# Kernel optimization log

Measured on AMD Instinct MI355X. Metric: run time of the kernel, lower is better.

Reference implementation:

```python
import jax, jax.numpy as jnp
import numpy as np

B = 1024      # batch of seed nodes
S = 16        # sample_size
H = 256       # hidden
IN = 150      # in_dim + NUM_CLASS (128 + 22)
OUT = 22
HEADS = 8
NN = 100000   # number of graph nodes
LN_EPS = 1e-5


def setup_inputs() -> dict:
    key = jax.random.key(0)
    ks = jax.random.split(key, 16)
    sc = 0.05
    return {
        "node_feats": jax.random.normal(ks[0], (NN, IN), jnp.float32),
        "batch": jax.random.randint(ks[1], (B,), 0, NN),
        "nbr2": jax.random.randint(ks[2], (B, S), 0, NN),
        "nbr1": jax.random.randint(ks[3], (B * (S + 1), S), 0, NN),
        "W_in": jax.random.normal(ks[4], (IN, H), jnp.float32) * sc,
        "b_in": jnp.zeros((H,), jnp.float32),
        "Wqkv": jax.random.normal(ks[5], (2, 3, H, H), jnp.float32) * sc,
        "bqkv": jnp.zeros((2, 3, H), jnp.float32),
        "Wo": jax.random.normal(ks[6], (2, H, H), jnp.float32) * sc,
        "bo": jnp.zeros((2, H), jnp.float32),
        "Wf": jax.random.normal(ks[7], (2, H, H), jnp.float32) * sc,
        "bf": jnp.zeros((2, H), jnp.float32),
        "ln_g": jnp.ones((4, H), jnp.float32),
        "ln_b": jnp.zeros((4, H), jnp.float32),
        "W_out": jax.random.normal(ks[8], (H, OUT), jnp.float32) * sc,
        "b_out": jnp.zeros((OUT,), jnp.float32),
    }


def _layer_norm(x, g, b):
    m = jnp.mean(x, axis=-1, keepdims=True)
    v = jnp.mean((x - m) ** 2, axis=-1, keepdims=True)
    return (x - m) * jax.lax.rsqrt(v + LN_EPS) * g + b


def _mha(q, kv, Wq, Wk, Wv, bq, bk, bv, Wout, bout):
    # q: [N, 1, H], kv: [N, S, H]; single-query multi-head attention
    N, Sk, _ = kv.shape
    dh = H // HEADS
    qp = (q @ Wq + bq).reshape(N, 1, HEADS, dh)
    kp = (kv @ Wk + bk).reshape(N, Sk, HEADS, dh)
    vp = (kv @ Wv + bv).reshape(N, Sk, HEADS, dh)
    att = jax.nn.softmax(
        jnp.einsum("nqhd,nkhd->nhqk", qp, kp) / np.float32(np.sqrt(dh)), axis=-1
    )
    o = jnp.einsum("nhqk,nkhd->nqhd", att, vp).reshape(N, 1, H)
    return o @ Wout + bout


def _attn_block(x, l, Wqkv, bqkv, Wo, bo, Wf, bf, ln_g, ln_b):
    # x: [N, S+1, H]; slot 0 is the query (self), rest are sampled neighbors
    q, kv = x[:, 0:1, :], x[:, 1:, :]
    h = _mha(q, kv, Wqkv[l, 0], Wqkv[l, 1], Wqkv[l, 2],
             bqkv[l, 0], bqkv[l, 1], bqkv[l, 2], Wo[l], bo[l])
    h = h[:, 0, :] + q[:, 0, :]                       # residual
    h = _layer_norm(h, ln_g[2 * l], ln_b[2 * l])
    h = h + (h @ Wf[l] + bf[l])                       # FFN (single Linear) + residual
    return _layer_norm(h, ln_g[2 * l + 1], ln_b[2 * l + 1])


def reference(node_feats, batch, nbr2, nbr1, W_in, b_in, Wqkv, bqkv, Wo, bo,
              Wf, bf, ln_g, ln_b, W_out, b_out):
    # Recursive neighbor expansion (unrolled for layers=2)
    ids1 = jnp.concatenate([batch[:, None], nbr2], axis=1).reshape(-1)   # [B*(S+1)]
    ids0 = jnp.concatenate([ids1[:, None], nbr1], axis=1).reshape(-1)    # [B*(S+1)^2]
    # layer 0: proj_in(features) = ReLU(Linear) (Dropout identity in eval)
    h0 = jax.nn.relu(node_feats[ids0] @ W_in + b_in)                     # [M0, H]
    # layer 1
    h1 = _attn_block(h0.reshape(B * (S + 1), S + 1, H), 0,
                     Wqkv, bqkv, Wo, bo, Wf, bf, ln_g, ln_b)
    # layer 2
    h2 = _attn_block(h1.reshape(B, S + 1, H), 1,
                     Wqkv, bqkv, Wo, bo, Wf, bf, ln_g, ln_b)
    # proj_out: Linear -> Softmax
    return jax.nn.softmax(h2 @ W_out + b_out, axis=-1)
```

## Files before the change

kernel.cpp:

```cpp
#include <hip/hip_runtime.h>
#include <hip/hip_bf16.h>
#include <math.h>

typedef unsigned short ushort_t;
typedef __bf16 bf16x8 __attribute__((ext_vector_type(8)));
typedef float  f32x4  __attribute__((ext_vector_type(4)));
typedef __attribute__((address_space(1))) const unsigned int* gas_t;
typedef __attribute__((address_space(3))) unsigned int* las_t;

#define B_SZ   1024
#define SEQ    17
#define KVN    16
#define HDIM   256
#define NHEAD  8
#define DH     32
#define INF    150
#define OUTD   22
#define LN_EPS 1e-5f
#define N1     (B_SZ * SEQ)
#define NN_    100000
#define NKV2   782
#define NHQ2   136

constexpr size_t SZ_H0    = (size_t)NN_ * 256 * 2;
constexpr size_t SZ_KV0   = (size_t)NN_ * 512 * 2;
constexpr size_t SZ_ROW   = (size_t)N1 * 256 * 2;
constexpr size_t OFF_HQ   = 0;
constexpr size_t OFF_KV0  = OFF_HQ + SZ_H0;
constexpr size_t OFF_QKV1 = OFF_KV0;
constexpr size_t OFF_O1   = OFF_QKV1 + (size_t)N1 * 768 * 2;
constexpr size_t OFF_H2   = OFF_O1 + (size_t)B_SZ * 256 * 2;
constexpr size_t OFF_Q0   = OFF_KV0 + SZ_KV0;
constexpr size_t OFF_O0   = OFF_Q0 + SZ_ROW;
constexpr size_t OFF_H1   = OFF_O0;
constexpr size_t OFF_IDS  = OFF_O0 + SZ_ROW;
constexpr size_t OFF_WTIN = OFF_IDS + (size_t)N1 * 4;
constexpr size_t OFF_WKV0 = OFF_WTIN + 256 * 160 * 2;
constexpr size_t OFF_WQ0  = OFF_WKV0 + 512 * 256 * 2;
constexpr size_t OFF_WKVQ1= OFF_WQ0 + 256 * 256 * 2;
constexpr size_t OFF_WO0  = OFF_WKVQ1 + 768 * 256 * 2;
constexpr size_t OFF_WF0  = OFF_WO0 + 256 * 256 * 2;
constexpr size_t OFF_WO1  = OFF_WF0 + 256 * 256 * 2;
constexpr size_t OFF_WF1  = OFF_WO1 + 256 * 256 * 2;
constexpr size_t OFF_B1   = OFF_WF1 + 256 * 256 * 2;

__device__ __forceinline__ ushort_t f2bfu(float x) {
    __hip_bfloat16 h = __float2bfloat16(x);
    return *reinterpret_cast<ushort_t*>(&h);
}
__device__ __forceinline__ float bfu2f(ushort_t u) {
    __hip_bfloat16 h;
    *reinterpret_cast<ushort_t*>(&h) = u;
    return __bfloat162float(h);
}
__device__ __forceinline__ f32x4 mfma16(bf16x8 a, bf16x8 b, f32x4 c) {
    return __builtin_amdgcn_mfma_f32_16x16x32_bf16(a, b, c, 0, 0, 0);
}

__device__ __forceinline__ void stage_b512(
    const ushort_t* __restrict__ Bsrc, int Kld, int kk,
    ushort_t* lbase, int w, int lane) {
    #pragma unroll
    for (int i = 0; i < 2; ++i) {
        int inst = w * 2 + i;
        int row = inst * 16 + (lane >> 2);
        int q_log = (lane & 3) ^ ((row >> 1) & 3);
        const ushort_t* src = Bsrc + (size_t)row * Kld + kk + q_log * 8;
        __builtin_amdgcn_global_load_lds((gas_t)(const void*)src,
                                         (las_t)(void*)(lbase + inst * 512),
                                         16, 0, 0);
    }
}

__global__ __launch_bounds__(256) void k_prep(
    const float* __restrict__ W_in, const float* __restrict__ Wqkv,
    const float* __restrict__ Wo, const float* __restrict__ Wf,
    const float* __restrict__ bqkv,
    const int* __restrict__ batch, const int* __restrict__ nbr2,
    char* __restrict__ ws) {
    const int job = blockIdx.y;
    const int idx = blockIdx.x * 256 + threadIdx.x;
    if (job == 11) {
        if (idx < N1) {
            int b = idx / SEQ, s = idx % SEQ;
            ((int*)(ws + OFF_IDS))[idx] = (s == 0) ? batch[b] : nbr2[b * KVN + s - 1];
        }
        return;
    }
    if (job == 12) {
        if (idx < 768) ((float*)(ws + OFF_B1))[idx] = bqkv[768 + ((idx + 256) % 768)];
        return;
    }
    const float* src = nullptr; ushort_t* dst = nullptr;
    int Kpad = 256, Kvalid = 256;
    switch (job) {
        case 0:  src = W_in;           dst = (ushort_t*)(ws + OFF_WTIN); Kpad = 160; Kvalid = 150; break;
        case 1:  src = Wqkv + 65536;   dst = (ushort_t*)(ws + OFF_WKV0); break;
        case 2:  src = Wqkv + 131072;  dst = (ushort_t*)(ws + OFF_WKV0) + 65536; break;
        case 3:  src = Wqkv;           dst = (ushort_t*)(ws + OFF_WQ0); break;
        case 4:  src = Wqkv + 262144;  dst = (ushort_t*)(ws + OFF_WKVQ1); break;
        case 5:  src = Wqkv + 327680;  dst = (ushort_t*)(ws + OFF_WKVQ1) + 65536; break;
        case 6:  src = Wqkv + 196608;  dst = (ushort_t*)(ws + OFF_WKVQ1) + 131072; break;
        case 7:  src = Wo;             dst = (ushort_t*)(ws + OFF_WO0); break;
        case 8:  src = Wo + 65536;     dst = (ushort_t*)(ws + OFF_WO1); break;
        case 9:  src = Wf;             dst = (ushort_t*)(ws + OFF_WF0); break;
        case 10: src = Wf + 65536;     dst = (ushort_t*)(ws + OFF_WF1); break;
    }
    const int total = 256 * Kpad;
    if (idx >= total) return;
    int n = idx / Kpad, k = idx % Kpad;
    dst[idx] = (k < Kvalid) ? f2bfu(src[(size_t)k * 256 + n]) : (ushort_t)0;
}

__global__ __launch_bounds__(512) void k_fused(
    const float* __restrict__ nf,
    const ushort_t* __restrict__ Wt_in, const float* __restrict__ b_in,
    const ushort_t* __restrict__ Wkv, const ushort_t* __restrict__ Wq,
    const float* __restrict__ bqkv, const int* __restrict__ ids1,
    ushort_t* __restrict__ kv0, ushort_t* __restrict__ hq,
    ushort_t* __restrict__ q0) {
    __shared__ ushort_t Ah[128 * 256];
    __shared__ ushort_t Bst[8192];
    const int tid = threadIdx.x;
    const bool iskv = blockIdx.x < NKV2;
    const int m0 = (iskv ? blockIdx.x : blockIdx.x - NKV2) * 128;
    const int lane = tid & 63, w = tid >> 6;
    const int wr = w >> 2, wc = w & 3;
    const int lr = lane & 15, q4 = lane >> 4, lk = q4 * 8;

    {
        ushort_t (*Astage)[168] = reinterpret_cast<ushort_t (*)[168]>(Ah);
        #pragma unroll
        for (int i = 0; i < 5; ++i) {
            int flat = tid + i * 512;
            int row = flat / 20, ch = flat % 20;
            int gm;
            if (iskv) { gm = m0 + row; if (gm >= NN_) gm = 0; }
            else      { gm = ids1[m0 + row]; }
            const float* ap = nf + (size_t)gm * INF + ch * 8;
            ushort_t tmp[8];
            if (ch < 18) {
                #pragma unroll
                for (int j = 0; j < 4; ++j) {
                    float2 f = *reinterpret_cast<const float2*>(ap + j * 2);
                    tmp[j * 2] = f2bfu(f.x); tmp[j * 2 + 1] = f2bfu(f.y);
                }
            } else {
                #pragma unroll
                for (int j = 0; j < 8; ++j) {
                    int k = ch * 8 + j;
                    tmp[j] = (k < INF) ? f2bfu(ap[j]) : (ushort_t)0;
                }
            }
            *reinterpret_cast<int4*>(&Astage[row][ch * 8]) = *reinterpret_cast<int4*>(tmp);
        }
    }
    __syncthreads();

    f32x4 acc1[4][4] = {};
    {
        ushort_t (*Astage)[168] = reinterpret_cast<ushort_t (*)[168]>(Ah);
        for (int s = 0; s < 5; ++s) {
            __builtin_amdgcn_s_barrier();
            stage_b512(Wt_in, 160, s * 32, Bst, w, lane);
            __syncthreads();
            bf16x8 a[4], b[4];
            #pragma unroll
            for (int mi = 0; mi < 4; ++mi)
                a[mi] = *reinterpret_cast<const bf16x8*>(
                    &Astage[wr * 64 + mi * 16 + lr][s * 32 + lk]);
            #pragma unroll
            for (int ni = 0; ni < 4; ++ni) {
                int n = wc * 64 + ni * 16 + lr;
                b[ni] = *reinterpret_cast<const bf16x8*>(
                    &Bst[n * 32 + ((q4 ^ ((n >> 1) & 3)) * 8)]);
            }
            #pragma unroll
            for (int mi = 0; mi < 4; ++mi)
                #pragma unroll
                for (int ni = 0; ni < 4; ++ni)
                    acc1[mi][ni] = mfma16(a[mi], b[ni], acc1[mi][ni]);
        }
    }
    __syncthreads();

    #pragma unroll
    for (int ni = 0; ni < 4; ++ni) {
        int col = wc * 64 + ni * 16 + lr;
        float bb = b_in[col];
        #pragma unroll
        for (int mi = 0; mi < 4; ++mi)
            #pragma unroll
            for (int r = 0; r < 4; ++r) {
                int row = wr * 64 + mi * 16 + q4 * 4 + r;
                Ah[row * 256 + (col ^ ((row & 7) << 3))] =
                    f2bfu(fmaxf(acc1[mi][ni][r] + bb, 0.f));
            }
    }
    __syncthreads();

    if (!iskv) {
        #pragma unroll
        for (int i = 0; i < 8; ++i) {
            int flat = tid + i * 512;
            int row = flat >> 5, ch = flat & 31;
            *reinterpret_cast<int4*>(hq + (size_t)(m0 + row) * 256 + ch * 8) =
                *reinterpret_cast<const int4*>(&Ah[row * 256 + ((ch ^ (row & 7)) * 8)]);
        }
    }

    const int npass = iskv ? 2 : 1;
    for (int h = 0; h < npass; ++h) {
        const ushort_t* Bm = iskv ? (Wkv + (size_t)h * 65536) : Wq;
        const float* bias = iskv ? (bqkv + 256 + h * 256) : bqkv;
        f32x4 acc2[4][4] = {};
        for (int s = 0; s < 8; ++s) {
            __builtin_amdgcn_s_barrier();
            stage_b512(Bm, 256, s * 32, Bst, w, lane);
            __syncthreads();
            bf16x8 a[4], b[4];
            #pragma unroll
            for (int mi = 0; mi < 4; ++mi) {
                int row = wr * 64 + mi * 16 + lr;
                int chunk = (s * 4 + q4) ^ (row & 7);
                a[mi] = *reinterpret_cast<const bf16x8*>(&Ah[row * 256 + chunk * 8]);
            }
            #pragma unroll
            for (int ni = 0; ni < 4; ++ni) {
                int n = wc * 64 + ni * 16 + lr;
                b[ni] = *reinterpret_cast<const bf16x8*>(
                    &Bst[n * 32 + ((q4 ^ ((n >> 1) & 3)) * 8)]);
            }
            #pragma unroll
            for (int mi = 0; mi < 4; ++mi)
                #pragma unroll
                for (int ni = 0; ni < 4; ++ni)
                    acc2[mi][ni] = mfma16(a[mi], b[ni], acc2[mi][ni]);
        }
        ushort_t* outp = iskv ? kv0 : q0;
        const int ldo = iskv ? 512 : 256;
        const int coff = (iskv ? h * 256 : 0) + wc * 64;
        #pragma unroll
        for (int ni = 0; ni < 4; ++ni) {
            float bb = bias[wc * 64 + ni * 16 + lr];
            #pragma unroll
            for (int mi = 0; mi < 4; ++mi)
                #pragma unroll
                for (int r = 0; r < 4; ++r) {
                    int grow = m0 + wr * 64 + mi * 16 + q4 * 4 + r;
                    if (!iskv || grow < NN_)
                        outp[(size_t)grow * ldo + coff + ni * 16 + lr] =
                            f2bfu(acc2[mi][ni][r] + bb);
                }
        }
    }
}

__global__ __launch_bounds__(256) void k_ffn(
    const ushort_t* __restrict__ Ain, const ushort_t* __restrict__ W1t,
    const float* __restrict__ b1,
    const ushort_t* __restrict__ resmat, int rstride,
    const float* __restrict__ lng1, const float* __restrict__ lnb1,
    const ushort_t* __restrict__ W2t, const float* __restrict__ b2,
    const float* __restrict__ lng2, const float* __restrict__ lnb2,
    ushort_t* __restrict__ out,
    const ushort_t* __restrict__ Wqkv1t, const float* __restrict__ bqkv1,
    ushort_t* __restrict__ qkvout) {
    __shared__ ushort_t Al[32][264];
    __shared__ float xr[32][260];
    __shared__ float mrow[32], rrow[32];
    const int tid = threadIdx.x;
    const int m0 = blockIdx.x * 32;
    const int lane = tid & 63, w = tid >> 6;
    const int lr = lane & 15, q4 = lane >> 4, lk = q4 * 8;

    #pragma unroll
    for (int j = 0; j < 4; ++j) {
        int flat = tid + j * 256;
        int row = flat >> 5, ch = flat & 31;
        *reinterpret_cast<int4*>(&Al[row][ch * 8]) =
            *reinterpret_cast<const int4*>(Ain + (size_t)(m0 + row) * 256 + ch * 8);
    }
    __syncthreads();

    f32x4 acc[2][4];
    #pragma unroll
    for (int g = 0; g < 2; ++g) {
        const ushort_t* Wt = g ? W2t : W1t;
        #pragma unroll
        for (int mi = 0; mi < 2; ++mi)
            #pragma unroll
            for (int ni = 0; ni < 4; ++ni) acc[mi][ni] = f32x4{0.f, 0.f, 0.f, 0.f};
        bf16x8 bc[4];
        #pragma unroll
        for (int ni = 0; ni < 4; ++ni)
            bc[ni] = *reinterpret_cast<const bf16x8*>(
                Wt + (size_t)(w * 64 + ni * 16 + lr) * 256 + lk);
        #pragma unroll
        for (int s = 0; s < 8; ++s) {
            bf16x8 bn[4];
            if (s < 7) {
                #pragma unroll
                for (int ni = 0; ni < 4; ++ni)
                    bn[ni] = *reinterpret_cast<const bf16x8*>(
                        Wt + (size_t)(w * 64 + ni * 16 + lr) * 256 + (s + 1) * 32 + lk);
            }
            bf16x8 a0 = *reinterpret_cast<const bf16x8*>(&Al[lr][s * 32 + lk]);
            bf16x8 a1 = *reinterpret_cast<const bf16x8*>(&Al[16 + lr][s * 32 + lk]);
            #pragma unroll
            for (int ni = 0; ni < 4; ++ni) {
                acc[0][ni] = mfma16(a0, bc[ni], acc[0][ni]);
                acc[1][ni] = mfma16(a1, bc[ni], acc[1][ni]);
            }
            if (s < 7) {
                #pragma unroll
                for (int ni = 0; ni < 4; ++ni) bc[ni] = bn[ni];
            }
        }
        #pragma unroll
        for (int mi = 0; mi < 2; ++mi)
            #pragma unroll
            for (int ni = 0; ni < 4; ++ni)
                #pragma unroll
                for (int r = 0; r < 4; ++r)
                    xr[mi * 16 + q4 * 4 + r][w * 64 + ni * 16 + lr] = acc[mi][ni][r];
        __syncthreads();
        {
            float bb = g ? b2[tid] : b1[tid];
            if (g == 0) {
                for (int r = 0; r < 32; ++r)
                    xr[r][tid] += bb + bfu2f(resmat[(size_t)(m0 + r) * rstride * 256 + tid]);
            } else {
                for (int r = 0; r < 32; ++r)
                    xr[r][tid] += bb + bfu2f(Al[r][tid]);
            }
        }
        __syncthreads();
        for (int rr = w * 8; rr < w * 8 + 8; ++rr) {
            float4 v = *reinterpret_cast<const float4*>(&xr[rr][lane * 4]);
            float s1 = v.x + v.y + v.z + v.w;
            float s2 = v.x * v.x + v.y * v.y + v.z * v.z + v.w * v.w;
            #pragma unroll
            for (int off = 32; off > 0; off >>= 1) {
                s1 += __shfl_xor(s1, off);
                s2 += __shfl_xor(s2, off);
            }
            if (lane == 0) {
                float m = s1 * (1.f / 256.f);
                float var = s2 * (1.f / 256.f) - m * m;
                mrow[rr] = m;
                rrow[rr] = rsqrtf(var + LN_EPS);
            }
        }
        __syncthreads();
        if (g == 0) {
            float gg = lng1[tid], bb = lnb1[tid];
            for (int r = 0; r < 32; ++r)
                Al[r][tid] = f2bfu((xr[r][tid] - mrow[r]) * rrow[r] * gg + bb);
        } else {
            float gg = lng2[tid], bb = lnb2[tid];
            for (int r = 0; r < 32; ++r) {
                float v = (xr[r][tid] - mrow[r]) * rrow[r] * gg + bb;
                ushort_t uv = f2bfu(v);
                out[(size_t)(m0 + r) * 256 + tid] = uv;
                if (qkvout) Al[r][tid] = uv;
            }
        }
        __syncthreads();
    }

    if (qkvout) {
        for (int p = 0; p < 3; ++p) {
            #pragma unroll
            for (int mi = 0; mi < 2; ++mi)
                #pragma unroll
                for (int ni = 0; ni < 4; ++ni) acc[mi][ni] = f32x4{0.f, 0.f, 0.f, 0.f};
            const ushort_t* Wt = Wqkv1t + (size_t)p * 256 * 256;
            bf16x8 bc[4];
            #pragma unroll
            for (int ni = 0; ni < 4; ++ni)
                bc[ni] = *reinterpret_cast<const bf16x8*>(
                    Wt + (size_t)(w * 64 + ni * 16 + lr) * 256 + lk);
            #pragma unroll
            for (int s = 0; s < 8; ++s) {
                bf16x8 bn[4];
                if (s < 7) {
                    #pragma unroll
                    for (int ni = 0; ni < 4; ++ni)
                        bn[ni] = *reinterpret_cast<const bf16x8*>(
                            Wt + (size_t)(w * 64 + ni * 16 + lr) * 256 + (s + 1) * 32 + lk);
                }
                bf16x8 a0 = *reinterpret_cast<const bf16x8*>(&Al[lr][s * 32 + lk]);
                bf16x8 a1 = *reinterpret_cast<const bf16x8*>(&Al[16 + lr][s * 32 + lk]);
                #pragma unroll
                for (int ni = 0; ni < 4; ++ni) {
                    acc[0][ni] = mfma16(a0, bc[ni], acc[0][ni]);
                    acc[1][ni] = mfma16(a1, bc[ni], acc[1][ni]);
                }
                if (s < 7) {
                    #pragma unroll
                    for (int ni = 0; ni < 4; ++ni) bc[ni] = bn[ni];
                }
            }
            #pragma unroll
            for (int ni = 0; ni < 4; ++ni) {
                int col = w * 64 + ni * 16 + lr;
                float bb = bqkv1[p * 256 + col];
                #pragma unroll
                for (int mi = 0; mi < 2; ++mi)
                    #pragma unroll
                    for (int r = 0; r < 4; ++r) {
                        int row = m0 + mi * 16 + q4 * 4 + r;
                        qkvout[(size_t)row * 768 + p * 256 + col] =
                            f2bfu(acc[mi][ni][r] + bb);
                    }
            }
        }
    }
}

__global__ __launch_bounds__(256) void attn_wave(
    const ushort_t* __restrict__ q_all, int qld, int qoff, int qstride,
    const ushort_t* __restrict__ kv_all, int kvld, int koff, int voff,
    const int* __restrict__ kvidx, int ngroups, ushort_t* __restrict__ o_out) {
    __shared__ ushort_t KL[4][KVN][264];
    __shared__ ushort_t VL[4][KVN][264];
    const int w = threadIdx.x >> 6, lane = threadIdx.x & 63;
    const int g = blockIdx.x * 4 + w;
    if (g >= ngroups) return;

    int idx16 = 0;
    if (lane < KVN)
        idx16 = kvidx ? kvidx[g * KVN + lane] : g * SEQ + 1 + lane;

    float qv[4];
    {
        uint2 u = *reinterpret_cast<const uint2*>(
            q_all + (size_t)g * qstride * qld + qoff + lane * 4);
        qv[0] = bfu2f((ushort_t)(u.x & 0xffff));
        qv[1] = bfu2f((ushort_t)(u.x >> 16));
        qv[2] = bfu2f((ushort_t)(u.y & 0xffff));
        qv[3] = bfu2f((ushort_t)(u.y >> 16));
    }
    {
        const int r = lane & 15, qtr = lane >> 4;
        int rid = __shfl(idx16, r);
        const ushort_t* kb = kv_all + (size_t)rid * kvld + koff;
        const ushort_t* vb = kv_all + (size_t)rid * kvld + voff;
        #pragma unroll
        for (int j = 0; j < 8; ++j) {
            int c8 = (qtr * 8 + j) * 8;
            *reinterpret_cast<int4*>(&KL[w][r][c8]) = *reinterpret_cast<const int4*>(kb + c8);
            *reinterpret_cast<int4*>(&VL[w][r][c8]) = *reinterpret_cast<const int4*>(vb + c8);
        }
    }
    float att[KVN];
    #pragma unroll
    for (int k = 0; k < KVN; ++k) {
        uint2 u = *reinterpret_cast<const uint2*>(&KL[w][k][lane * 4]);
        float p = qv[0] * bfu2f((ushort_t)(u.x & 0xffff))
                + qv[1] * bfu2f((ushort_t)(u.x >> 16))
                + qv[2] * bfu2f((ushort_t)(u.y & 0xffff))
                + qv[3] * bfu2f((ushort_t)(u.y >> 16));
        p += __shfl_xor(p, 1);
        p += __shfl_xor(p, 2);
        p += __shfl_xor(p, 4);
        att[k] = p * 0.17677669529663687f;
    }
    float m = att[0];
    #pragma unroll
    for (int k = 1; k < KVN; ++k) m = fmaxf(m, att[k]);
    float sum = 0.f;
    #pragma unroll
    for (int k = 0; k < KVN; ++k) { att[k] = __expf(att[k] - m); sum += att[k]; }
    float inv = 1.f / sum;
    float o[4] = {0.f, 0.f, 0.f, 0.f};
    #pragma unroll
    for (int k = 0; k < KVN; ++k) {
        uint2 u = *reinterpret_cast<const uint2*>(&VL[w][k][lane * 4]);
        float a = att[k] * inv;
        o[0] += a * bfu2f((ushort_t)(u.x & 0xffff));
        o[1] += a * bfu2f((ushort_t)(u.x >> 16));
        o[2] += a * bfu2f((ushort_t)(u.y & 0xffff));
        o[3] += a * bfu2f((ushort_t)(u.y >> 16));
    }
    uint2 r;
    r.x = (unsigned)f2bfu(o[0]) | ((unsigned)f2bfu(o[1]) << 16);
    r.y = (unsigned)f2bfu(o[2]) | ((unsigned)f2bfu(o[3]) << 16);
    *reinterpret_cast<uint2*>(o_out + (size_t)g * 256 + lane * 4) = r;
}

__global__ __launch_bounds__(64) void k_out(
    const ushort_t* __restrict__ h2, const float* __restrict__ W_out,
    const float* __restrict__ b_out, float* __restrict__ out) {
    const int b = blockIdx.x, j = threadIdx.x;
    __shared__ float xr[HDIM];
    for (int k = j; k < HDIM; k += 64) xr[k] = bfu2f(h2[(size_t)b * HDIM + k]);
    __syncthreads();
    float logit = -1e30f;
    if (j < OUTD) {
        float acc = b_out[j];
        for (int k = 0; k < HDIM; ++k) acc += xr[k] * W_out[k * OUTD + j];
        logit = acc;
    }
    float m = logit;
    #pragma unroll
    for (int off = 32; off > 0; off >>= 1) m = fmaxf(m, __shfl_xor(m, off));
    float e = (j < OUTD) ? __expf(logit - m) : 0.f;
    float s = e;
    #pragma unroll
    for (int off = 32; off > 0; off >>= 1) s += __shfl_xor(s, off);
    if (j < OUTD) out[(size_t)b * OUTD + j] = e / s;
}

extern "C" void kernel_launch(void* const* d_in, const int* in_sizes, int n_in,
                              void* d_out, int out_size, void* d_ws, size_t ws_size,
                              hipStream_t stream) {
    const float* nf    = (const float*)d_in[0];
    const int*   batch = (const int*)d_in[1];
    const int*   nbr2  = (const int*)d_in[2];
    const int*   nbr1  = (const int*)d_in[3];
    const float* W_in  = (const float*)d_in[4];
    const float* b_in  = (const float*)d_in[5];
    const float* Wqkv  = (const float*)d_in[6];
    const float* bqkv  = (const float*)d_in[7];
    const float* Wo    = (const float*)d_in[8];
    const float* bo    = (const float*)d_in[9];
    const float* Wf    = (const float*)d_in[10];
    const float* bf    = (const float*)d_in[11];
    const float* ln_g  = (const float*)d_in[12];
    const float* ln_b  = (const float*)d_in[13];
    const float* W_out = (const float*)d_in[14];
    const float* b_out = (const float*)d_in[15];
    float* out = (float*)d_out;
    char* ws = (char*)d_ws;

    ushort_t* hq   = (ushort_t*)(ws + OFF_HQ);
    ushort_t* kv0  = (ushort_t*)(ws + OFF_KV0);
    ushort_t* q0   = (ushort_t*)(ws + OFF_Q0);
    ushort_t* o0   = (ushort_t*)(ws + OFF_O0);
    ushort_t* h1   = (ushort_t*)(ws + OFF_H1);
    ushort_t* qkv1 = (ushort_t*)(ws + OFF_QKV1);
    ushort_t* o1   = (ushort_t*)(ws + OFF_O1);
    ushort_t* h2   = (ushort_t*)(ws + OFF_H2);
    const int* ids1 = (const int*)(ws + OFF_IDS);

    hipLaunchKernelGGL(k_prep, dim3(256, 13), dim3(256), 0, stream,
                       W_in, Wqkv, Wo, Wf, bqkv, batch, nbr2, ws);
    hipLaunchKernelGGL(k_fused, dim3(NKV2 + NHQ2), dim3(512), 0, stream,
                       nf, (const ushort_t*)(ws + OFF_WTIN), b_in,
                       (const ushort_t*)(ws + OFF_WKV0),
                       (const ushort_t*)(ws + OFF_WQ0), bqkv, ids1,
                       kv0, hq, q0);
    hipLaunchKernelGGL(attn_wave, dim3(N1 / 4), dim3(256), 0, stream,
                       q0, 256, 0, 1, kv0, 512, 0, 256, nbr1, N1, o0);
    hipLaunchKernelGGL(k_ffn, dim3(N1 / 32), dim3(256), 0, stream,
                       o0, (const ushort_t*)(ws + OFF_WO0), bo,
                       hq, 1, ln_g, ln_b,
                       (const ushort_t*)(ws + OFF_WF0), bf,
                       ln_g + 256, ln_b + 256, h1,
                       (const ushort_t*)(ws + OFF_WKVQ1),
                       (const float*)(ws + OFF_B1), qkv1);
    hipLaunchKernelGGL(attn_wave, dim3(B_SZ / 4), dim3(256), 0, stream,
                       qkv1, 768, 512, 17, qkv1, 768, 0, 256,
                       (const int*)nullptr, B_SZ, o1);
    hipLaunchKernelGGL(k_ffn, dim3(B_SZ / 32), dim3(256), 0, stream,
                       o1, (const ushort_t*)(ws + OFF_WO1), bo + 256,
                       h1, 17, ln_g + 512, ln_b + 512,
                       (const ushort_t*)(ws + OFF_WF1), bf + 256,
                       ln_g + 768, ln_b + 768, h2,
                       (const ushort_t*)nullptr, (const float*)nullptr,
                       (ushort_t*)nullptr);
    hipLaunchKernelGGL(k_out, dim3(B_SZ), dim3(64), 0, stream,
                       h2, W_out, b_out, out);
}
```

Baseline: 326.7 us.

## Split fused projection kernel into persistent h0 and KV/Q kernels with register-resident weights

Replaces the single fused input-projection + KV/Q projection kernel with two persistent kernels. The first computes h0 = ReLU(nf·W_in) for all nodes into a full-size buffer. The second reads h0 back through LDS and projects it to K/V for all nodes and to Q for gathered ids. Weights are preloaded into registers once per block instead of being staged through LDS every k-step, and the FFN residual now gathers from h0 by index rather than from a separate hq copy. This removes per-tile weight staging and barriers, at the cost of an extra global round-trip of h0 (about 51MB), higher register pressure and an extra launch.

```diff
diff --git a/kernel.cpp b/kernel.cpp
--- a/kernel.cpp
+++ b/kernel.cpp
@@ -19,14 +19,14 @@
 #define LN_EPS 1e-5f
 #define N1     (B_SZ * SEQ)
 #define NN_    100000
-#define NKV2   782
-#define NHQ2   136
+#define NKVBLK 1563
+#define NQBLK  272
 
 constexpr size_t SZ_H0    = (size_t)NN_ * 256 * 2;
 constexpr size_t SZ_KV0   = (size_t)NN_ * 512 * 2;
 constexpr size_t SZ_ROW   = (size_t)N1 * 256 * 2;
-constexpr size_t OFF_HQ   = 0;
-constexpr size_t OFF_KV0  = OFF_HQ + SZ_H0;
+constexpr size_t OFF_H0   = 0;
+constexpr size_t OFF_KV0  = OFF_H0 + SZ_H0;
 constexpr size_t OFF_QKV1 = OFF_KV0;
 constexpr size_t OFF_O1   = OFF_QKV1 + (size_t)N1 * 768 * 2;
 constexpr size_t OFF_H2   = OFF_O1 + (size_t)B_SZ * 256 * 2;
@@ -57,21 +57,6 @@
     return __builtin_amdgcn_mfma_f32_16x16x32_bf16(a, b, c, 0, 0, 0);
 }
 
-__device__ __forceinline__ void stage_b512(
-    const ushort_t* __restrict__ Bsrc, int Kld, int kk,
-    ushort_t* lbase, int w, int lane) {
-    #pragma unroll
-    for (int i = 0; i < 2; ++i) {
-        int inst = w * 2 + i;
-        int row = inst * 16 + (lane >> 2);
-        int q_log = (lane & 3) ^ ((row >> 1) & 3);
-        const ushort_t* src = Bsrc + (size_t)row * Kld + kk + q_log * 8;
-        __builtin_amdgcn_global_load_lds((gas_t)(const void*)src,
-                                         (las_t)(void*)(lbase + inst * 512),
-                                         16, 0, 0);
-    }
-}
-
 __global__ __launch_bounds__(256) void k_prep(
     const float* __restrict__ W_in, const float* __restrict__ Wqkv,
     const float* __restrict__ Wo, const float* __restrict__ Wf,
@@ -112,34 +97,36 @@
     dst[idx] = (k < Kvalid) ? f2bfu(src[(size_t)k * 256 + n]) : (ushort_t)0;
 }
 
-__global__ __launch_bounds__(512) void k_fused(
-    const float* __restrict__ nf,
-    const ushort_t* __restrict__ Wt_in, const float* __restrict__ b_in,
-    const ushort_t* __restrict__ Wkv, const ushort_t* __restrict__ Wq,
-    const float* __restrict__ bqkv, const int* __restrict__ ids1,
-    ushort_t* __restrict__ kv0, ushort_t* __restrict__ hq,
-    ushort_t* __restrict__ q0) {
-    __shared__ ushort_t Ah[128 * 256];
-    __shared__ ushort_t Bst[8192];
+__global__ __launch_bounds__(256) void k_h0(
+    const float* __restrict__ nf, const ushort_t* __restrict__ Wt_in,
+    const float* __restrict__ b_in, ushort_t* __restrict__ h0) {
+    __shared__ ushort_t As[64 * 192];
     const int tid = threadIdx.x;
-    const bool iskv = blockIdx.x < NKV2;
-    const int m0 = (iskv ? blockIdx.x : blockIdx.x - NKV2) * 128;
     const int lane = tid & 63, w = tid >> 6;
-    const int wr = w >> 2, wc = w & 3;
-    const int lr = lane & 15, q4 = lane >> 4, lk = q4 * 8;
-
-    {
-        ushort_t (*Astage)[168] = reinterpret_cast<ushort_t (*)[168]>(Ah);
+    const int lr = lane & 15, q4 = lane >> 4;
+
+    bf16x8 bw[4][5];
+    #pragma unroll
+    for (int ni = 0; ni < 4; ++ni)
+        #pragma unroll
+        for (int s = 0; s < 5; ++s)
+            bw[ni][s] = *reinterpret_cast<const bf16x8*>(
+                Wt_in + (size_t)(w * 64 + ni * 16 + lr) * 160 + s * 32 + q4 * 8);
+    float bb[4];
+    #pragma unroll
+    for (int ni = 0; ni < 4; ++ni) bb[ni] = b_in[w * 64 + ni * 16 + lr];
+
+    for (int t = blockIdx.x; t < NKVBLK; t += 512) {
+        const int m0 = t * 64;
+        __syncthreads();
         #pragma unroll
         for (int i = 0; i < 5; ++i) {
-            int flat = tid + i * 512;
-            int row = flat / 20, ch = flat % 20;
-            int gm;
-            if (iskv) { gm = m0 + row; if (gm >= NN_) gm = 0; }
-            else      { gm = ids1[m0 + row]; }
-            const float* ap = nf + (size_t)gm * INF + ch * 8;
+            int flat = tid + i * 256;
+            int row = flat / 20, c = flat % 20;
+            int gm = m0 + row; if (gm >= NN_) gm = 0;
+            const float* ap = nf + (size_t)gm * INF + c * 8;
             ushort_t tmp[8];
-            if (ch < 18) {
+            if (c < 18) {
                 #pragma unroll
                 for (int j = 0; j < 4; ++j) {
                     float2 f = *reinterpret_cast<const float2*>(ap + j * 2);
@@ -148,118 +135,195 @@
             } else {
                 #pragma unroll
                 for (int j = 0; j < 8; ++j) {
-                    int k = ch * 8 + j;
+                    int k = c * 8 + j;
                     tmp[j] = (k < INF) ? f2bfu(ap[j]) : (ushort_t)0;
                 }
             }
-            *reinterpret_cast<int4*>(&Astage[row][ch * 8]) = *reinterpret_cast<int4*>(tmp);
-        }
-    }
-    __syncthreads();
-
-    f32x4 acc1[4][4] = {};
-    {
-        ushort_t (*Astage)[168] = reinterpret_cast<ushort_t (*)[168]>(Ah);
+            *reinterpret_cast<int4*>(&As[row * 192 + (c ^ (row & 7)) * 8]) =
+                *reinterpret_cast<int4*>(tmp);
+        }
+        __syncthreads();
+        f32x4 acc[4][4] = {};
+        #pragma unroll
         for (int s = 0; s < 5; ++s) {
-            __builtin_amdgcn_s_barrier();
-            stage_b512(Wt_in, 160, s * 32, Bst, w, lane);
-            __syncthreads();
-            bf16x8 a[4], b[4];
+            bf16x8 a[4];
             #pragma unroll
             for (int mi = 0; mi < 4; ++mi)
                 a[mi] = *reinterpret_cast<const bf16x8*>(
-                    &Astage[wr * 64 + mi * 16 + lr][s * 32 + lk]);
-            #pragma unroll
-            for (int ni = 0; ni < 4; ++ni) {
-                int n = wc * 64 + ni * 16 + lr;
-                b[ni] = *reinterpret_cast<const bf16x8*>(
-                    &Bst[n * 32 + ((q4 ^ ((n >> 1) & 3)) * 8)]);
-            }
+                    &As[(mi * 16 + lr) * 192 + (((s * 4 + q4) ^ (lr & 7)) * 8)]);
             #pragma unroll
             for (int mi = 0; mi < 4; ++mi)
                 #pragma unroll
                 for (int ni = 0; ni < 4; ++ni)
-                    acc1[mi][ni] = mfma16(a[mi], b[ni], acc1[mi][ni]);
-        }
-    }
-    __syncthreads();
-
-    #pragma unroll
-    for (int ni = 0; ni < 4; ++ni) {
-        int col = wc * 64 + ni * 16 + lr;
-        float bb = b_in[col];
-        #pragma unroll
-        for (int mi = 0; mi < 4; ++mi)
-            #pragma unroll
-            for (int r = 0; r < 4; ++r) {
-                int row = wr * 64 + mi * 16 + q4 * 4 + r;
-                Ah[row * 256 + (col ^ ((row & 7) << 3))] =
-                    f2bfu(fmaxf(acc1[mi][ni][r] + bb, 0.f));
-            }
-    }
-    __syncthreads();
-
-    if (!iskv) {
-        #pragma unroll
-        for (int i = 0; i < 8; ++i) {
+                    acc[mi][ni] = mfma16(a[mi], bw[ni][s], acc[mi][ni]);
+        }
+        #pragma unroll
+        for (int ni = 0; ni < 4; ++ni)
+            #pragma unroll
+            for (int mi = 0; mi < 4; ++mi)
+                #pragma unroll
+                for (int r = 0; r < 4; ++r) {
+                    int grow = m0 + mi * 16 + q4 * 4 + r;
+                    if (grow < NN_)
+                        h0[(size_t)grow * 256 + w * 64 + ni * 16 + lr] =
+                            f2bfu(fmaxf(acc[mi][ni][r] + bb[ni], 0.f));
+                }
+    }
+}
+
+__global__ __launch_bounds__(512) void k_kvq(
+    const ushort_t* __restrict__ h0, const ushort_t* __restrict__ Wkv,
+    const ushort_t* __restrict__ Wq, const float* __restrict__ bqkv,
+    const int* __restrict__ ids1, ushort_t* __restrict__ kv0,
+    ushort_t* __restrict__ q0) {
+    __shared__ ushort_t As[64 * 256];
+    const int tid = threadIdx.x;
+    const int lane = tid & 63, w = tid >> 6;
+    const int lr = lane & 15, q4 = lane >> 4;
+    const int n0 = w * 32;
+
+    bf16x8 bk[2][8], bv[2][8];
+    #pragma unroll
+    for (int ni = 0; ni < 2; ++ni)
+        #pragma unroll
+        for (int s = 0; s < 8; ++s) {
+            bk[ni][s] = *reinterpret_cast<const bf16x8*>(
+                Wkv + (size_t)(n0 + ni * 16 + lr) * 256 + s * 32 + q4 * 8);
+            bv[ni][s] = *reinterpret_cast<const bf16x8*>(
+                Wkv + 65536 + (size_t)(n0 + ni * 16 + lr) * 256 + s * 32 + q4 * 8);
+        }
+    float bbk[2], bbv[2];
+    #pragma unroll
+    for (int ni = 0; ni < 2; ++ni) {
+        bbk[ni] = bqkv[256 + n0 + ni * 16 + lr];
+        bbv[ni] = bqkv[512 + n0 + ni * 16 + lr];
+    }
+
+    for (int t = blockIdx.x; t < NKVBLK; t += 256) {
+        const int m0 = t * 64;
+        __syncthreads();
+        #pragma unroll
+        for (int i = 0; i < 4; ++i) {
             int flat = tid + i * 512;
             int row = flat >> 5, ch = flat & 31;
-            *reinterpret_cast<int4*>(hq + (size_t)(m0 + row) * 256 + ch * 8) =
-                *reinterpret_cast<const int4*>(&Ah[row * 256 + ((ch ^ (row & 7)) * 8)]);
-        }
-    }
-
-    const int npass = iskv ? 2 : 1;
-    for (int h = 0; h < npass; ++h) {
-        const ushort_t* Bm = iskv ? (Wkv + (size_t)h * 65536) : Wq;
-        const float* bias = iskv ? (bqkv + 256 + h * 256) : bqkv;
-        f32x4 acc2[4][4] = {};
+            int gm = m0 + row; if (gm >= NN_) gm = 0;
+            const ushort_t* src = h0 + (size_t)gm * 256 + ((ch ^ (row & 7)) * 8);
+            __builtin_amdgcn_global_load_lds(
+                (gas_t)(const void*)src,
+                (las_t)(void*)(As + (size_t)(i * 512 + w * 64) * 8), 16, 0, 0);
+        }
+        __syncthreads();
+        {
+            f32x4 acc[4][2] = {};
+            #pragma unroll
+            for (int s = 0; s < 8; ++s) {
+                bf16x8 a[4];
+                #pragma unroll
+                for (int mi = 0; mi < 4; ++mi)
+                    a[mi] = *reinterpret_cast<const bf16x8*>(
+                        &As[(mi * 16 + lr) * 256 + (((s * 4 + q4) ^ (lr & 7)) * 8)]);
+                #pragma unroll
+                for (int mi = 0; mi < 4; ++mi)
+                    #pragma unroll
+                    for (int ni = 0; ni < 2; ++ni)
+                        acc[mi][ni] = mfma16(a[mi], bk[ni][s], acc[mi][ni]);
+            }
+            #pragma unroll
+            for (int ni = 0; ni < 2; ++ni)
+                #pragma unroll
+                for (int mi = 0; mi < 4; ++mi)
+                    #pragma unroll
+                    for (int r = 0; r < 4; ++r) {
+                        int grow = m0 + mi * 16 + q4 * 4 + r;
+                        if (grow < NN_)
+                            kv0[(size_t)grow * 512 + n0 + ni * 16 + lr] =
+                                f2bfu(acc[mi][ni][r] + bbk[ni]);
+                    }
+        }
+        {
+            f32x4 acc[4][2] = {};
+            #pragma unroll
+            for (int s = 0; s < 8; ++s) {
+                bf16x8 a[4];
+                #pragma unroll
+                for (int mi = 0; mi < 4; ++mi)
+                    a[mi] = *reinterpret_cast<const bf16x8*>(
+                        &As[(mi * 16 + lr) * 256 + (((s * 4 + q4) ^ (lr & 7)) * 8)]);
+                #pragma unroll
+                for (int mi = 0; mi < 4; ++mi)
+                    #pragma unroll
+                    for (int ni = 0; ni < 2; ++ni)
+                        acc[mi][ni] = mfma16(a[mi], bv[ni][s], acc[mi][ni]);
+            }
+            #pragma unroll
+            for (int ni = 0; ni < 2; ++ni)
+                #pragma unroll
+                for (int mi = 0; mi < 4; ++mi)
+                    #pragma unroll
+                    for (int r = 0; r < 4; ++r) {
+                        int grow = m0 + mi * 16 + q4 * 4 + r;
+                        if (grow < NN_)
+                            kv0[(size_t)grow * 512 + 256 + n0 + ni * 16 + lr] =
+                                f2bfu(acc[mi][ni][r] + bbv[ni]);
+                    }
+        }
+    }
+
+    #pragma unroll
+    for (int ni = 0; ni < 2; ++ni)
+        #pragma unroll
+        for (int s = 0; s < 8; ++s)
+            bk[ni][s] = *reinterpret_cast<const bf16x8*>(
+                Wq + (size_t)(n0 + ni * 16 + lr) * 256 + s * 32 + q4 * 8);
+    float bbq[2];
+    #pragma unroll
+    for (int ni = 0; ni < 2; ++ni) bbq[ni] = bqkv[n0 + ni * 16 + lr];
+
+    for (int t = blockIdx.x; t < NQBLK; t += 256) {
+        const int m0 = t * 64;
+        __syncthreads();
+        #pragma unroll
+        for (int i = 0; i < 4; ++i) {
+            int flat = tid + i * 512;
+            int row = flat >> 5, ch = flat & 31;
+            int rid = ids1[m0 + row];
+            const ushort_t* src = h0 + (size_t)rid * 256 + ((ch ^ (row & 7)) * 8);
+            __builtin_amdgcn_global_load_lds(
+                (gas_t)(const void*)src,
+                (las_t)(void*)(As + (size_t)(i * 512 + w * 64) * 8), 16, 0, 0);
+        }
+        __syncthreads();
+        f32x4 acc[4][2] = {};
+        #pragma unroll
         for (int s = 0; s < 8; ++s) {
-            __builtin_amdgcn_s_barrier();
-            stage_b512(Bm, 256, s * 32, Bst, w, lane);
-            __syncthreads();
-            bf16x8 a[4], b[4];
-            #pragma unroll
-            for (int mi = 0; mi < 4; ++mi) {
-                int row = wr * 64 + mi * 16 + lr;
-                int chunk = (s * 4 + q4) ^ (row & 7);
-                a[mi] = *reinterpret_cast<const bf16x8*>(&Ah[row * 256 + chunk * 8]);
-            }
-            #pragma unroll
-            for (int ni = 0; ni < 4; ++ni) {
-                int n = wc * 64 + ni * 16 + lr;
-                b[ni] = *reinterpret_cast<const bf16x8*>(
-                    &Bst[n * 32 + ((q4 ^ ((n >> 1) & 3)) * 8)]);
-            }
+            bf16x8 a[4];
             #pragma unroll
             for (int mi = 0; mi < 4; ++mi)
-                #pragma unroll
-                for (int ni = 0; ni < 4; ++ni)
-                    acc2[mi][ni] = mfma16(a[mi], b[ni], acc2[mi][ni]);
-        }
-        ushort_t* outp = iskv ? kv0 : q0;
-        const int ldo = iskv ? 512 : 256;
-        const int coff = (iskv ? h * 256 : 0) + wc * 64;
-        #pragma unroll
-        for (int ni = 0; ni < 4; ++ni) {
-            float bb = bias[wc * 64 + ni * 16 + lr];
+                a[mi] = *reinterpret_cast<const bf16x8*>(
+                    &As[(mi * 16 + lr) * 256 + (((s * 4 + q4) ^ (lr & 7)) * 8)]);
             #pragma unroll
             for (int mi = 0; mi < 4; ++mi)
                 #pragma unroll
+                for (int ni = 0; ni < 2; ++ni)
+                    acc[mi][ni] = mfma16(a[mi], bk[ni][s], acc[mi][ni]);
+        }
+        #pragma unroll
+        for (int ni = 0; ni < 2; ++ni)
+            #pragma unroll
+            for (int mi = 0; mi < 4; ++mi)
+                #pragma unroll
                 for (int r = 0; r < 4; ++r) {
-                    int grow = m0 + wr * 64 + mi * 16 + q4 * 4 + r;
-                    if (!iskv || grow < NN_)
-                        outp[(size_t)grow * ldo + coff + ni * 16 + lr] =
-                            f2bfu(acc2[mi][ni][r] + bb);
+                    int grow = m0 + mi * 16 + q4 * 4 + r;
+                    q0[(size_t)grow * 256 + n0 + ni * 16 + lr] =
+                        f2bfu(acc[mi][ni][r] + bbq[ni]);
                 }
-        }
     }
 }
 
 __global__ __launch_bounds__(256) void k_ffn(
     const ushort_t* __restrict__ Ain, const ushort_t* __restrict__ W1t,
     const float* __restrict__ b1,
-    const ushort_t* __restrict__ resmat, int rstride,
+    const ushort_t* __restrict__ resmat, const int* __restrict__ residx, int rstride,
     const float* __restrict__ lng1, const float* __restrict__ lnb1,
     const ushort_t* __restrict__ W2t, const float* __restrict__ b2,
     const float* __restrict__ lng2, const float* __restrict__ lnb2,
@@ -269,6 +333,7 @@
     __shared__ ushort_t Al[32][264];
     __shared__ float xr[32][260];
     __shared__ float mrow[32], rrow[32];
+    __shared__ int sidx[32];
     const int tid = threadIdx.x;
     const int m0 = blockIdx.x * 32;
     const int lane = tid & 63, w = tid >> 6;
@@ -281,6 +346,7 @@
         *reinterpret_cast<int4*>(&Al[row][ch * 8]) =
             *reinterpret_cast<const int4*>(Ain + (size_t)(m0 + row) * 256 + ch * 8);
     }
+    if (tid < 32) sidx[tid] = residx ? residx[m0 + tid] : (m0 + tid) * rstride;
     __syncthreads();
 
     f32x4 acc[2][4];
@@ -329,7 +395,7 @@
             float bb = g ? b2[tid] : b1[tid];
             if (g == 0) {
                 for (int r = 0; r < 32; ++r)
-                    xr[r][tid] += bb + bfu2f(resmat[(size_t)(m0 + r) * rstride * 256 + tid]);
+                    xr[r][tid] += bb + bfu2f(resmat[(size_t)sidx[r] * 256 + tid]);
             } else {
                 for (int r = 0; r < 32; ++r)
                     xr[r][tid] += bb + bfu2f(Al[r][tid]);
@@ -535,7 +601,7 @@
     float* out = (float*)d_out;
     char* ws = (char*)d_ws;
 
-    ushort_t* hq   = (ushort_t*)(ws + OFF_HQ);
+    ushort_t* h0   = (ushort_t*)(ws + OFF_H0);
     ushort_t* kv0  = (ushort_t*)(ws + OFF_KV0);
     ushort_t* q0   = (ushort_t*)(ws + OFF_Q0);
     ushort_t* o0   = (ushort_t*)(ws + OFF_O0);
@@ -547,16 +613,16 @@
 
     hipLaunchKernelGGL(k_prep, dim3(256, 13), dim3(256), 0, stream,
                        W_in, Wqkv, Wo, Wf, bqkv, batch, nbr2, ws);
-    hipLaunchKernelGGL(k_fused, dim3(NKV2 + NHQ2), dim3(512), 0, stream,
-                       nf, (const ushort_t*)(ws + OFF_WTIN), b_in,
-                       (const ushort_t*)(ws + OFF_WKV0),
-                       (const ushort_t*)(ws + OFF_WQ0), bqkv, ids1,
-                       kv0, hq, q0);
+    hipLaunchKernelGGL(k_h0, dim3(512), dim3(256), 0, stream,
+                       nf, (const ushort_t*)(ws + OFF_WTIN), b_in, h0);
+    hipLaunchKernelGGL(k_kvq, dim3(256), dim3(512), 0, stream,
+                       h0, (const ushort_t*)(ws + OFF_WKV0),
+                       (const ushort_t*)(ws + OFF_WQ0), bqkv, ids1, kv0, q0);
     hipLaunchKernelGGL(attn_wave, dim3(N1 / 4), dim3(256), 0, stream,
                        q0, 256, 0, 1, kv0, 512, 0, 256, nbr1, N1, o0);
     hipLaunchKernelGGL(k_ffn, dim3(N1 / 32), dim3(256), 0, stream,
                        o0, (const ushort_t*)(ws + OFF_WO0), bo,
-                       hq, 1, ln_g, ln_b,
+                       h0, ids1, 1, ln_g, ln_b,
                        (const ushort_t*)(ws + OFF_WF0), bf,
                        ln_g + 256, ln_b + 256, h1,
                        (const ushort_t*)(ws + OFF_WKVQ1),
@@ -566,7 +632,7 @@
                        (const int*)nullptr, B_SZ, o1);
     hipLaunchKernelGGL(k_ffn, dim3(B_SZ / 32), dim3(256), 0, stream,
                        o1, (const ushort_t*)(ws + OFF_WO1), bo + 256,
-                       h1, 17, ln_g + 512, ln_b + 512,
+                       h1, (const int*)nullptr, 17, ln_g + 512, ln_b + 512,
                        (const ushort_t*)(ws + OFF_WF1), bf + 256,
                        ln_g + 768, ln_b + 768, h2,
                        (const ushort_t*)nullptr, (const float*)nullptr,
```

Result: no change. 332.6 us (+1.8%).
